# Optimization experiments

Hardware: AMD Instinct MI355X
Metric: run time of the kernel (lower is better)

Reference implementation:

```python
import jax, jax.numpy as jnp
import numpy as np

WINDOW = 1024


def _dft_weights(window):
    # w[k, n] = exp(-2*pi*i*k*n/window); torch module stores real/imag parts as conv weights
    n = np.arange(window)
    ang = -2.0 * np.pi * (n[:, None] * n[None, :]) / window  # [K, N] in float64 like numpy
    return np.cos(ang).astype(np.float32), np.sin(ang).astype(np.float32)


def setup_inputs() -> dict:
    key = jax.random.key(0)
    k1, k2, k3, k4 = jax.random.split(key, 4)
    w_real, w_imag = _dft_weights(WINDOW)
    bound = 1.0 / np.sqrt(WINDOW)  # torch Conv1d default bias init: U(-1/sqrt(fan_in), 1/sqrt(fan_in))
    return {
        "x_r": jax.random.normal(k1, (8, 4096, WINDOW), dtype=jnp.float32),
        "x_i": jax.random.normal(k2, (8, 4096, WINDOW), dtype=jnp.float32),
        "w_real": jnp.asarray(w_real),
        "w_imag": jnp.asarray(w_imag),
        "b_real": jax.random.uniform(k3, (WINDOW,), minval=-bound, maxval=bound, dtype=jnp.float32),
        "b_imag": jax.random.uniform(k4, (WINDOW,), minval=-bound, maxval=bound, dtype=jnp.float32),
    }


def reference(x_r, x_i, w_real, w_imag, b_real, b_imag):
    # Conv1d with full-window kernel == matmul over the last axis.
    # conv_real(x) = x @ w_real.T + b_real ; conv_imag(x) = x @ w_imag.T + b_imag
    xr_wr = jnp.einsum('bfn,kn->bfk', x_r, w_real)
    xr_wi = jnp.einsum('bfn,kn->bfk', x_r, w_imag)
    xi_wr = jnp.einsum('bfn,kn->bfk', x_i, w_real)
    xi_wi = jnp.einsum('bfn,kn->bfk', x_i, w_imag)
    real = (xr_wr + b_real) - (xi_wi + b_imag)
    imag = (xr_wi + b_imag) + (xi_wr + b_real)
    return (real, imag)
```

## Files before the change

kernel.cpp:

```cpp
#include <hip/hip_runtime.h>
#include <stdint.h>

#define NFFT  1024
#define MROWS 32768
#define GRID  2048

__device__ __forceinline__ int P(int i) { return i + (i >> 4); }

__device__ __forceinline__ void dft4(float& ar, float& ai, float& br_, float& bi_,
                                     float& cr, float& ci, float& dr, float& di) {
  const float t0r = ar + cr,  t0i = ai + ci;
  const float t1r = ar - cr,  t1i = ai - ci;
  const float t2r = br_ + dr, t2i = bi_ + di;
  const float t3r = bi_ - di, t3i = dr - br_;
  ar  = t0r + t2r; ai  = t0i + t2i;
  br_ = t1r + t3r; bi_ = t1i + t3i;
  cr  = t0r - t2r; ci  = t0i - t2i;
  dr  = t1r - t3r; di  = t1i - t3i;
}

__device__ __forceinline__ void cmul(float& xr, float& xi, float c, float s) {
  const float r = xr * c - xi * s;
  xi = xr * s + xi * c;
  xr = r;
}

__global__ void __launch_bounds__(256, 3)
fft1024(const float* __restrict__ xr, const float* __restrict__ xi,
        const float* __restrict__ wr, const float* __restrict__ wi,
        const float* __restrict__ br, const float* __restrict__ bi,
        float* __restrict__ out) {
  __shared__ __align__(16) float twr[1088], twi[1088];
  __shared__ __align__(16) float lds[4 * 2176];

  const int tid = threadIdx.x;
  const int w   = tid >> 6;
  const int t   = tid & 63;
  float* buf = lds + w * 2176;
  const int b  = t & 15;
  const int a  = t >> 4;
  const int t4 = t << 2;

  {
    const float4 cr = *(const float4*)(wr + NFFT + 4 * tid);
    const float4 ci = *(const float4*)(wi + NFFT + 4 * tid);
    twr[P(4 * tid + 0)] = cr.x; twr[P(4 * tid + 1)] = cr.y;
    twr[P(4 * tid + 2)] = cr.z; twr[P(4 * tid + 3)] = cr.w;
    twi[P(4 * tid + 0)] = ci.x; twi[P(4 * tid + 1)] = ci.y;
    twi[P(4 * tid + 2)] = ci.z; twi[P(4 * tid + 3)] = ci.w;
  }
  __syncthreads();

  float badd_r[4][4], badd_i[4][4];
#pragma unroll
  for (int k = 0; k < 4; ++k) {
    const float4 fb = *(const float4*)(br + t4 + 256 * k);
    const float4 gb = *(const float4*)(bi + t4 + 256 * k);
    badd_r[k][0] = fb.x - gb.x; badd_i[k][0] = fb.x + gb.x;
    badd_r[k][1] = fb.y - gb.y; badd_i[k][1] = fb.y + gb.y;
    badd_r[k][2] = fb.z - gb.z; badd_i[k][2] = fb.z + gb.z;
    badd_r[k][3] = fb.w - gb.w; badd_i[k][3] = fb.w + gb.w;
  }

#pragma unroll 1
  for (int row = blockIdx.x * 4 + w; row < MROWS; row += GRID * 4) {
    const float* pr = xr + (size_t)row * NFFT;
    const float* px = xi + (size_t)row * NFFT;

    float vr[16], vi[16];
#pragma unroll
    for (int e = 0; e < 16; ++e) { vr[e] = pr[t + 64 * e]; vi[e] = px[t + 64 * e]; }

#pragma unroll
    for (int q = 0; q < 4; ++q)
      dft4(vr[q], vi[q], vr[q + 4], vi[q + 4], vr[q + 8], vi[q + 8], vr[q + 12], vi[q + 12]);

#pragma unroll
    for (int m = 1; m < 4; ++m)
#pragma unroll
      for (int q = 1; q < 4; ++q)
        cmul(vr[q + 4 * m], vi[q + 4 * m], twr[P(64 * q * m)], twi[P(64 * q * m)]);
#pragma unroll
    for (int m = 0; m < 4; ++m)
      dft4(vr[4 * m], vi[4 * m], vr[1 + 4 * m], vi[1 + 4 * m],
           vr[2 + 4 * m], vi[2 + 4 * m], vr[3 + 4 * m], vi[3 + 4 * m]);

#pragma unroll
    for (int u = 0; u < 16; ++u) {
      const int m = u & 3, k1 = u >> 2;
      *(float2*)&buf[2 * P(16 * t + u)] = make_float2(vr[k1 + 4 * m], vi[k1 + 4 * m]);
    }
    asm volatile("" ::: "memory");

#pragma unroll
    for (int q = 0; q < 4; ++q)
#pragma unroll
      for (int r = 0; r < 4; ++r) {
        const float2 f = *(const float2*)&buf[2 * P(t + 64 * q + 256 * r)];
        vr[q + 4 * r] = f.x; vi[q + 4 * r] = f.y;
      }
    asm volatile("" ::: "memory");
    {
      float c2[4], s2[4];
#pragma unroll
      for (int r = 1; r < 4; ++r) { c2[r] = twr[P(16 * r * b)]; s2[r] = twi[P(16 * r * b)]; }
#pragma unroll
      for (int q = 0; q < 4; ++q) {
#pragma unroll
        for (int r = 1; r < 4; ++r)
          cmul(vr[q + 4 * r], vi[q + 4 * r], c2[r], s2[r]);
        dft4(vr[q], vi[q], vr[q + 4], vi[q + 4], vr[q + 8], vi[q + 8], vr[q + 12], vi[q + 12]);
      }
    }

#pragma unroll
    for (int k2 = 0; k2 < 4; ++k2) {
#pragma unroll
      for (int q = 1; q < 4; ++q) {
        const int e = 4 * q * (b + 16 * k2);
        cmul(vr[q + 4 * k2], vi[q + 4 * k2], twr[P(e)], twi[P(e)]);
      }
      dft4(vr[4 * k2], vi[4 * k2], vr[1 + 4 * k2], vi[1 + 4 * k2],
           vr[2 + 4 * k2], vi[2 + 4 * k2], vr[3 + 4 * k2], vi[3 + 4 * k2]);
    }

#pragma unroll
    for (int k2 = 0; k2 < 4; ++k2)
#pragma unroll
      for (int k3 = 0; k3 < 4; ++k3)
        *(float2*)&buf[2 * P(256 * a + b + 16 * k2 + 64 * k3)] =
            make_float2(vr[k3 + 4 * k2], vi[k3 + 4 * k2]);
    asm volatile("" ::: "memory");

#pragma unroll
    for (int m = 0; m < 4; ++m)
#pragma unroll
      for (int r = 0; r < 4; ++r) {
        const float2 f = *(const float2*)&buf[2 * P(t4 + m + 256 * r)];
        vr[m + 4 * r] = f.x; vi[m + 4 * r] = f.y;
      }
    asm volatile("" ::: "memory");
#pragma unroll
    for (int m = 0; m < 4; ++m) {
#pragma unroll
      for (int r = 1; r < 4; ++r) {
        const int e = r * (t4 + m);
        cmul(vr[m + 4 * r], vi[m + 4 * r], twr[P(e)], twi[P(e)]);
      }
      dft4(vr[m], vi[m], vr[m + 4], vi[m + 4], vr[m + 8], vi[m + 8], vr[m + 12], vi[m + 12]);
    }

    float* o_r = out + (size_t)row * NFFT;
    float* o_i = out + (size_t)MROWS * NFFT + (size_t)row * NFFT;
#pragma unroll
    for (int k = 0; k < 4; ++k) {
      float4 R, I;
      R.x = vr[0 + 4 * k] + badd_r[k][0]; I.x = vi[0 + 4 * k] + badd_i[k][0];
      R.y = vr[1 + 4 * k] + badd_r[k][1]; I.y = vi[1 + 4 * k] + badd_i[k][1];
      R.z = vr[2 + 4 * k] + badd_r[k][2]; I.z = vi[2 + 4 * k] + badd_i[k][2];
      R.w = vr[3 + 4 * k] + badd_r[k][3]; I.w = vi[3 + 4 * k] + badd_i[k][3];
      *(float4*)(o_r + t4 + 256 * k) = R;
      *(float4*)(o_i + t4 + 256 * k) = I;
    }
  }
}

extern "C" void kernel_launch(void* const* d_in, const int* in_sizes, int n_in,
                              void* d_out, int out_size, void* d_ws, size_t ws_size,
                              hipStream_t stream) {
  const float* xr = (const float*)d_in[0];
  const float* xi = (const float*)d_in[1];
  const float* wr = (const float*)d_in[2];
  const float* wi = (const float*)d_in[3];
  const float* br = (const float*)d_in[4];
  const float* bi = (const float*)d_in[5];
  float* out = (float*)d_out;
  (void)in_sizes; (void)n_in; (void)out_size; (void)d_ws; (void)ws_size;

  fft1024<<<GRID, 256, 0, stream>>>(xr, xi, wr, wi, br, bi, out);
}
```

Measured before the change: 560.8 us.

## Shrink twiddle table, derive higher twiddles by recurrence, raise occupancy

Replaces the 1024-entry padded twiddle table in LDS with a 256-entry unpadded table. Higher-power twiddles are now computed on the fly by complex squaring and multiplication, and the first-stage twiddles are held as scalar constants. The per-thread precombined bias registers are dropped in favour of reloading the bias in the store loop, and launch bounds move from 3 to 4 blocks per CU. The aim is to cut LDS and register pressure so more waves can hide memory latency. The cost is extra FLOPs, slight rounding differences from the recurrence, and redundant bias reloads on every row.

```diff
diff --git a/kernel.cpp b/kernel.cpp
--- a/kernel.cpp
+++ b/kernel.cpp
@@ -25,12 +25,12 @@
   xr = r;
 }
 
-__global__ void __launch_bounds__(256, 3)
+__global__ void __launch_bounds__(256, 4)
 fft1024(const float* __restrict__ xr, const float* __restrict__ xi,
         const float* __restrict__ wr, const float* __restrict__ wi,
         const float* __restrict__ br, const float* __restrict__ bi,
         float* __restrict__ out) {
-  __shared__ __align__(16) float twr[1088], twi[1088];
+  __shared__ __align__(16) float twr[256], twi[256];
   __shared__ __align__(16) float lds[4 * 2176];
 
   const int tid = threadIdx.x;
@@ -41,26 +41,16 @@
   const int a  = t >> 4;
   const int t4 = t << 2;
 
-  {
-    const float4 cr = *(const float4*)(wr + NFFT + 4 * tid);
-    const float4 ci = *(const float4*)(wi + NFFT + 4 * tid);
-    twr[P(4 * tid + 0)] = cr.x; twr[P(4 * tid + 1)] = cr.y;
-    twr[P(4 * tid + 2)] = cr.z; twr[P(4 * tid + 3)] = cr.w;
-    twi[P(4 * tid + 0)] = ci.x; twi[P(4 * tid + 1)] = ci.y;
-    twi[P(4 * tid + 2)] = ci.z; twi[P(4 * tid + 3)] = ci.w;
-  }
+  twr[tid] = wr[NFFT + tid];
+  twi[tid] = wi[NFFT + tid];
   __syncthreads();
 
-  float badd_r[4][4], badd_i[4][4];
-#pragma unroll
-  for (int k = 0; k < 4; ++k) {
-    const float4 fb = *(const float4*)(br + t4 + 256 * k);
-    const float4 gb = *(const float4*)(bi + t4 + 256 * k);
-    badd_r[k][0] = fb.x - gb.x; badd_i[k][0] = fb.x + gb.x;
-    badd_r[k][1] = fb.y - gb.y; badd_i[k][1] = fb.y + gb.y;
-    badd_r[k][2] = fb.z - gb.z; badd_i[k][2] = fb.z + gb.z;
-    badd_r[k][3] = fb.w - gb.w; badd_i[k][3] = fb.w + gb.w;
-  }
+  const float u1r = wr[NFFT +  64], u1i = wi[NFFT +  64];
+  const float u2r = wr[NFFT + 128], u2i = wi[NFFT + 128];
+  const float u3r = wr[NFFT + 192], u3i = wi[NFFT + 192];
+  const float u4r = wr[NFFT + 256], u4i = wi[NFFT + 256];
+  const float u6r = wr[NFFT + 384], u6i = wi[NFFT + 384];
+  const float u9r = wr[NFFT + 576], u9i = wi[NFFT + 576];
 
 #pragma unroll 1
   for (int row = blockIdx.x * 4 + w; row < MROWS; row += GRID * 4) {
@@ -69,17 +59,23 @@
 
     float vr[16], vi[16];
 #pragma unroll
-    for (int e = 0; e < 16; ++e) { vr[e] = pr[t + 64 * e]; vi[e] = px[t + 64 * e]; }
+    for (int q = 0; q < 4; ++q)
+#pragma unroll
+      for (int r = 0; r < 4; ++r) {
+        vr[q + 4 * r] = pr[t + 64 * (q + 4 * r)];
+        vi[q + 4 * r] = px[t + 64 * (q + 4 * r)];
+      }
 
 #pragma unroll
     for (int q = 0; q < 4; ++q)
       dft4(vr[q], vi[q], vr[q + 4], vi[q + 4], vr[q + 8], vi[q + 8], vr[q + 12], vi[q + 12]);
 
-#pragma unroll
-    for (int m = 1; m < 4; ++m)
-#pragma unroll
-      for (int q = 1; q < 4; ++q)
-        cmul(vr[q + 4 * m], vi[q + 4 * m], twr[P(64 * q * m)], twi[P(64 * q * m)]);
+    cmul(vr[5],  vi[5],  u1r, u1i);  cmul(vr[6],  vi[6],  u2r, u2i);
+    cmul(vr[7],  vi[7],  u3r, u3i);
+    cmul(vr[9],  vi[9],  u2r, u2i);  cmul(vr[10], vi[10], u4r, u4i);
+    cmul(vr[11], vi[11], u6r, u6i);
+    cmul(vr[13], vi[13], u3r, u3i);  cmul(vr[14], vi[14], u6r, u6i);
+    cmul(vr[15], vi[15], u9r, u9i);
 #pragma unroll
     for (int m = 0; m < 4; ++m)
       dft4(vr[4 * m], vi[4 * m], vr[1 + 4 * m], vi[1 + 4 * m],
@@ -101,25 +97,26 @@
       }
     asm volatile("" ::: "memory");
     {
-      float c2[4], s2[4];
-#pragma unroll
-      for (int r = 1; r < 4; ++r) { c2[r] = twr[P(16 * r * b)]; s2[r] = twi[P(16 * r * b)]; }
+      const float c1 = twr[16 * b], s1 = twi[16 * b];
+      const float c2 = c1 * c1 - s1 * s1, s2 = 2.f * c1 * s1;
+      const float c3 = c2 * c1 - s2 * s1, s3 = c2 * s1 + s2 * c1;
 #pragma unroll
       for (int q = 0; q < 4; ++q) {
-#pragma unroll
-        for (int r = 1; r < 4; ++r)
-          cmul(vr[q + 4 * r], vi[q + 4 * r], c2[r], s2[r]);
+        cmul(vr[q + 4],  vi[q + 4],  c1, s1);
+        cmul(vr[q + 8],  vi[q + 8],  c2, s2);
+        cmul(vr[q + 12], vi[q + 12], c3, s3);
         dft4(vr[q], vi[q], vr[q + 4], vi[q + 4], vr[q + 8], vi[q + 8], vr[q + 12], vi[q + 12]);
       }
     }
 
 #pragma unroll
     for (int k2 = 0; k2 < 4; ++k2) {
-#pragma unroll
-      for (int q = 1; q < 4; ++q) {
-        const int e = 4 * q * (b + 16 * k2);
-        cmul(vr[q + 4 * k2], vi[q + 4 * k2], twr[P(e)], twi[P(e)]);
-      }
+      const float c1 = twr[4 * (b + 16 * k2)], s1 = twi[4 * (b + 16 * k2)];
+      const float c2 = c1 * c1 - s1 * s1, s2 = 2.f * c1 * s1;
+      const float c3 = c2 * c1 - s2 * s1, s3 = c2 * s1 + s2 * c1;
+      cmul(vr[1 + 4 * k2], vi[1 + 4 * k2], c1, s1);
+      cmul(vr[2 + 4 * k2], vi[2 + 4 * k2], c2, s2);
+      cmul(vr[3 + 4 * k2], vi[3 + 4 * k2], c3, s3);
       dft4(vr[4 * k2], vi[4 * k2], vr[1 + 4 * k2], vi[1 + 4 * k2],
            vr[2 + 4 * k2], vi[2 + 4 * k2], vr[3 + 4 * k2], vi[3 + 4 * k2]);
     }
@@ -140,25 +137,34 @@
         vr[m + 4 * r] = f.x; vi[m + 4 * r] = f.y;
       }
     asm volatile("" ::: "memory");
+    {
+      const float4 C = *(const float4*)&twr[t4];
+      const float4 S = *(const float4*)&twi[t4];
+      const float cc[4] = {C.x, C.y, C.z, C.w};
+      const float ss[4] = {S.x, S.y, S.z, S.w};
 #pragma unroll
-    for (int m = 0; m < 4; ++m) {
-#pragma unroll
-      for (int r = 1; r < 4; ++r) {
-        const int e = r * (t4 + m);
-        cmul(vr[m + 4 * r], vi[m + 4 * r], twr[P(e)], twi[P(e)]);
+      for (int m = 0; m < 4; ++m) {
+        const float c1 = cc[m], s1 = ss[m];
+        const float c2 = c1 * c1 - s1 * s1, s2 = 2.f * c1 * s1;
+        const float c3 = c2 * c1 - s2 * s1, s3 = c2 * s1 + s2 * c1;
+        cmul(vr[m + 4],  vi[m + 4],  c1, s1);
+        cmul(vr[m + 8],  vi[m + 8],  c2, s2);
+        cmul(vr[m + 12], vi[m + 12], c3, s3);
+        dft4(vr[m], vi[m], vr[m + 4], vi[m + 4], vr[m + 8], vi[m + 8], vr[m + 12], vi[m + 12]);
       }
-      dft4(vr[m], vi[m], vr[m + 4], vi[m + 4], vr[m + 8], vi[m + 8], vr[m + 12], vi[m + 12]);
     }
 
     float* o_r = out + (size_t)row * NFFT;
     float* o_i = out + (size_t)MROWS * NFFT + (size_t)row * NFFT;
 #pragma unroll
     for (int k = 0; k < 4; ++k) {
+      const float4 fb = *(const float4*)(br + t4 + 256 * k);
+      const float4 gb = *(const float4*)(bi + t4 + 256 * k);
       float4 R, I;
-      R.x = vr[0 + 4 * k] + badd_r[k][0]; I.x = vi[0 + 4 * k] + badd_i[k][0];
-      R.y = vr[1 + 4 * k] + badd_r[k][1]; I.y = vi[1 + 4 * k] + badd_i[k][1];
-      R.z = vr[2 + 4 * k] + badd_r[k][2]; I.z = vi[2 + 4 * k] + badd_i[k][2];
-      R.w = vr[3 + 4 * k] + badd_r[k][3]; I.w = vi[3 + 4 * k] + badd_i[k][3];
+      R.x = vr[0 + 4 * k] + fb.x - gb.x; I.x = vi[0 + 4 * k] + fb.x + gb.x;
+      R.y = vr[1 + 4 * k] + fb.y - gb.y; I.y = vi[1 + 4 * k] + fb.y + gb.y;
+      R.z = vr[2 + 4 * k] + fb.z - gb.z; I.z = vi[2 + 4 * k] + fb.z + gb.z;
+      R.w = vr[3 + 4 * k] + fb.w - gb.w; I.w = vi[3 + 4 * k] + fb.w + gb.w;
       *(float4*)(o_r + t4 + 256 * k) = R;
       *(float4*)(o_i + t4 + 256 * k) = I;
     }
```

Result: faster. 492.2 us (-12.2%).
